# Kernel optimization log

Hardware: AMD Instinct MI355X
Metric: run time of the kernel (lower is better)

Reference implementation:

```python
import jax, jax.numpy as jnp
import numpy as np

# Grid config: output_shape = [2, 40, 400, 352, 16] -> sparse_shape = [41, 400, 352]
B, Dz, Hy, Wx = 2, 41, 400, 352
N_PER = 20000          # active voxels per sample
C_IN = 128
# Strided SparseConv3d(k=3, s=2, p=1) output spatial dims
Do, Ho, Wo = (Dz + 2 - 3) // 2 + 1, (Hy + 2 - 3) // 2 + 1, (Wx + 2 - 3) // 2 + 1


def setup_inputs() -> dict:
    rng = np.random.default_rng(0)
    coors_list = []
    for b in range(B):
        # unique voxel positions per sample (z limited to original 40-deep grid)
        flat = rng.choice((Dz - 1) * Hy * Wx, size=N_PER, replace=False)
        z = flat // (Hy * Wx)
        r = flat % (Hy * Wx)
        y = r // Wx
        x = r % Wx
        coors_list.append(np.stack([np.full(N_PER, b), z, y, x], axis=1))
    coors = jnp.asarray(np.concatenate(coors_list, 0), jnp.int32)  # [N,4]

    key = jax.random.key(0)
    k1, k2, k3, k4 = jax.random.split(key, 4)
    N = B * N_PER
    voxel_features = jax.random.normal(k1, (N, C_IN), jnp.float32)
    W1 = jax.random.normal(k2, (3, 3, 3, C_IN, 16), jnp.float32) * (1.0 / np.sqrt(27 * C_IN))
    W2 = jax.random.normal(k3, (3, 3, 3, 16, 16), jnp.float32) * (1.0 / np.sqrt(27 * 16))
    W3 = jax.random.normal(k4, (3, 3, 3, 16, 32), jnp.float32) * (1.0 / np.sqrt(27 * 16))
    return dict(voxel_features=voxel_features, coors=coors, W1=W1, W2=W2, W3=W3, batch_size=B)


def _offsets():
    o = jnp.stack(jnp.meshgrid(jnp.arange(3), jnp.arange(3), jnp.arange(3), indexing='ij'), -1)
    return o.reshape(27, 3)  # [27,3] kernel taps


def reference(voxel_features, coors, W1, W2, W3, batch_size):
    N = voxel_features.shape[0]
    offs = _offsets()

    # --- rulebook: dense index grid, padded by 1 so neighbor lookups never go OOB
    grid = jnp.full((batch_size, Dz + 2, Hy + 2, Wx + 2), -1, jnp.int32)
    grid = grid.at[coors[:, 0], coors[:, 1] + 1, coors[:, 2] + 1, coors[:, 3] + 1].set(
        jnp.arange(N, dtype=jnp.int32))
    # neighbor voxel index for every active site and every 3x3x3 tap: [N,27]
    nbr = grid[coors[:, 0:1], coors[:, 1:2] + offs[:, 0], coors[:, 2:3] + offs[:, 1],
               coors[:, 3:4] + offs[:, 2]]
    valid = (nbr >= 0)[..., None]
    nbr_c = jnp.clip(nbr, 0, N - 1)

    def subm(feat, W):  # submanifold conv: gather -> GEMM, output only on active sites
        Cin, Cout = W.shape[3], W.shape[4]
        g = jnp.where(valid, feat[nbr_c], 0.0)                      # [N,27,Cin]
        return jnp.einsum('nkc,kcd->nd', g, W.reshape(27, Cin, Cout))

    x = jax.nn.relu(subm(voxel_features, W1))   # SubMConv3d(128->16) + ReLU
    x = jax.nn.relu(subm(x, W2))                # SubMConv3d(16->16, same rulebook) + ReLU

    # --- SparseConv3d(16->32, k=3, stride=2, pad=1): scatter-add into downsampled grid
    contrib = jnp.einsum('nc,kcd->nkd', x, W3.reshape(27, 16, 32))  # [N,27,32]
    oz = coors[:, 1:2] + 1 - offs[:, 0]  # p_in + pad - k, must be even and in range
    oy = coors[:, 2:3] + 1 - offs[:, 1]
    ox = coors[:, 3:4] + 1 - offs[:, 2]
    pz, py, px = oz // 2, oy // 2, ox // 2
    ok = ((oz % 2 == 0) & (oy % 2 == 0) & (ox % 2 == 0) &
          (pz >= 0) & (pz < Do) & (py >= 0) & (py < Ho) & (px >= 0) & (px < Wo))
    total = batch_size * Do * Ho * Wo
    flat = coors[:, 0:1] * (Do * Ho * Wo) + pz * (Ho * Wo) + py * Wo + px
    flat = jnp.where(ok, flat, total)  # invalid -> dummy slot
    out = jnp.zeros((total + 1, 32), x.dtype).at[flat.reshape(-1)].add(
        contrib.reshape(-1, 32))[:total]
    out = jax.nn.relu(out).reshape(batch_size, Do, Ho, Wo, 32)  # dense() of sparse output
    return out
```

## Files before the change

### kernel.cpp

```cpp
#include <hip/hip_runtime.h>

#define B_   2
#define DZ   41
#define HY   400
#define WX   352
#define NVOX 40000
#define PD   43
#define PH   402
#define PW   354
#define DO_  21
#define HO_  200
#define WO_  176
#define C1   128
#define GRID_CELLS (B_*PD*PH*PW)
#define OUT_POS    (B_*DO_*HO_*WO_)
#define OUT_BYTES  ((size_t)OUT_POS * 32 * sizeof(float))


__global__ void k_build(const int* __restrict__ coors, unsigned short* __restrict__ grid) {
    int n = blockIdx.x * blockDim.x + threadIdx.x;
    if (n >= NVOX) return;
    int b = coors[4*n+0], z = coors[4*n+1], y = coors[4*n+2], x = coors[4*n+3];
    grid[((b*PD + z+1)*PH + y+1)*PW + x+1] = (unsigned short)(n + 1);
}

__global__ void k_nbr(const int* __restrict__ coors, const unsigned short* __restrict__ grid,
                      int* __restrict__ list, int* __restrict__ cnt) {
    int n = blockIdx.x * blockDim.x + threadIdx.x;
    if (n >= NVOX) return;
    int b = coors[4*n+0], z = coors[4*n+1], y = coors[4*n+2], x = coors[4*n+3];
    int c = 0;
    int* lp = list + n * 27;
    #pragma unroll
    for (int dz = 0; dz < 3; ++dz) {
        #pragma unroll
        for (int dy = 0; dy < 3; ++dy) {
            const unsigned short* row = grid + ((size_t)(b*PD + z + dz)*PH + (y + dy))*PW + x;
            #pragma unroll
            for (int dx = 0; dx < 3; ++dx) {
                int id = (int)row[dx] - 1;
                if (id >= 0) lp[c++] = ((dz*9 + dy*3 + dx) << 16) | id;
            }
        }
    }
    cnt[n] = c;
}

__global__ void k_subm1(const float* __restrict__ feat,
                        const float* __restrict__ W1,
                        const int* __restrict__ list, const int* __restrict__ cnt,
                        float* __restrict__ x1) {
    __shared__ int s_list[16][28];
    __shared__ int s_cnt[16];
    int base = blockIdx.x * 16;
    if (threadIdx.x < 16) {
        int n = base + threadIdx.x;
        s_cnt[threadIdx.x] = (n < NVOX) ? cnt[n] : 0;
    }
    for (int i = threadIdx.x; i < 16*27; i += 256) {
        int v = i / 27, k = i % 27;
        int n = base + v;
        s_list[v][k] = (n < NVOX) ? list[n*27 + k] : 0;
    }
    __syncthreads();
    int v = threadIdx.x >> 4, d = threadIdx.x & 15;
    int n = base + v;
    if (n >= NVOX) return;
    int m = s_cnt[v];
    float a0 = 0.f, a1 = 0.f, a2 = 0.f, a3 = 0.f;
    for (int t = 0; t < m; ++t) {
        int e = s_list[v][t];
        int k = e >> 16, idx = e & 0xFFFF;
        const float4* f4 = (const float4*)(feat + (size_t)idx * C1);
        const float* w = W1 + k * (C1*16) + d;
        #pragma unroll
        for (int c4 = 0; c4 < 32; ++c4) {
            float4 fv = f4[c4];
            const float* wp = w + c4 * 64;
            a0 += fv.x * wp[0];
            a1 += fv.y * wp[16];
            a2 += fv.z * wp[32];
            a3 += fv.w * wp[48];
        }
    }
    x1[n*16 + d] = fmaxf((a0 + a1) + (a2 + a3), 0.f);
}

__global__ void k_subm2(const float* __restrict__ x1,
                        const float* __restrict__ W2,
                        const int* __restrict__ list, const int* __restrict__ cnt,
                        float* __restrict__ x2) {
    __shared__ int   s_list[16][28];
    __shared__ int   s_cnt[16];
    __shared__ float s_w2[27*16*16];
    for (int i = threadIdx.x; i < 27*16*16; i += 256) s_w2[i] = W2[i];
    int base = blockIdx.x * 16;
    if (threadIdx.x < 16) {
        int n = base + threadIdx.x;
        s_cnt[threadIdx.x] = (n < NVOX) ? cnt[n] : 0;
    }
    for (int i = threadIdx.x; i < 16*27; i += 256) {
        int v = i / 27, k = i % 27;
        int n = base + v;
        s_list[v][k] = (n < NVOX) ? list[n*27 + k] : 0;
    }
    __syncthreads();
    int v = threadIdx.x >> 4, d = threadIdx.x & 15;
    int n = base + v;
    if (n >= NVOX) return;
    int m = s_cnt[v];
    float a0 = 0.f, a1 = 0.f, a2 = 0.f, a3 = 0.f;
    for (int t = 0; t < m; ++t) {
        int e = s_list[v][t];
        int k = e >> 16, idx = e & 0xFFFF;
        const float4* x4 = (const float4*)(x1 + (size_t)idx * 16);
        float4 xa = x4[0], xb = x4[1], xc = x4[2], xd = x4[3];
        const float* wp = s_w2 + k * 256 + d;
        a0 += xa.x * wp[0*16]  + xa.y * wp[1*16]  + xa.z * wp[2*16]  + xa.w * wp[3*16];
        a1 += xb.x * wp[4*16]  + xb.y * wp[5*16]  + xb.z * wp[6*16]  + xb.w * wp[7*16];
        a2 += xc.x * wp[8*16]  + xc.y * wp[9*16]  + xc.z * wp[10*16] + xc.w * wp[11*16];
        a3 += xd.x * wp[12*16] + xd.y * wp[13*16] + xd.z * wp[14*16] + xd.w * wp[15*16];
    }
    x2[n*16 + d] = fmaxf((a0 + a1) + (a2 + a3), 0.f);
}

__device__ __forceinline__ int axis_taps(int pcoord, int outdim, int* ds, int* ps) {
    if (pcoord & 1) { ds[0] = 1; ps[0] = pcoord >> 1; return 1; }
    int h = pcoord >> 1, nu = 0;
    if (h < outdim) { ds[nu] = 0; ps[nu] = h; nu++; }
    ds[nu] = 2; ps[nu] = h - 1; nu++;
    return nu;
}

__global__ void k_scatter(const float* __restrict__ x2,
                          const float* __restrict__ W3,
                          const int* __restrict__ coors,
                          float* __restrict__ out) {
    int v = threadIdx.x >> 5, d = threadIdx.x & 31;
    int n = blockIdx.x * 8 + v;
    if (n >= NVOX) return;
    int b  = coors[4*n+0];
    int zp = coors[4*n+1] + 1, yp = coors[4*n+2] + 1, xp = coors[4*n+3] + 1;
    int dz[2], pz[2], dy[2], py[2], dx[2], px[2];
    int nz = axis_taps(zp, DO_, dz, pz);
    int ny = axis_taps(yp, HO_, dy, py);
    int nx = axis_taps(xp, WO_, dx, px);
    const float4* xr = (const float4*)(x2 + (size_t)n * 16);
    float r[16];
    *(float4*)(r + 0)  = xr[0];
    *(float4*)(r + 4)  = xr[1];
    *(float4*)(r + 8)  = xr[2];
    *(float4*)(r + 12) = xr[3];
    int bofs = b * (DO_*HO_*WO_);
    for (int iz = 0; iz < nz; ++iz)
        for (int iy = 0; iy < ny; ++iy)
            for (int ix = 0; ix < nx; ++ix) {
                int k = dz[iz]*9 + dy[iy]*3 + dx[ix];
                int p = bofs + (pz[iz]*HO_ + py[iy])*WO_ + px[ix];
                const float* w = W3 + k*512 + d;
                float acc = 0.f;
                #pragma unroll
                for (int c = 0; c < 16; ++c) acc += r[c] * w[c * 32];
                atomicAdd(out + (size_t)p * 32 + d, acc);
            }
}

__global__ void k_relu(const int* __restrict__ coors, float* __restrict__ out) {
    int v = threadIdx.x >> 5, d = threadIdx.x & 31;
    int n = blockIdx.x * 8 + v;
    if (n >= NVOX) return;
    int b  = coors[4*n+0];
    int zp = coors[4*n+1] + 1, yp = coors[4*n+2] + 1, xp = coors[4*n+3] + 1;
    int dz[2], pz[2], dy[2], py[2], dx[2], px[2];
    int nz = axis_taps(zp, DO_, dz, pz);
    int ny = axis_taps(yp, HO_, dy, py);
    int nx = axis_taps(xp, WO_, dx, px);
    int bofs = b * (DO_*HO_*WO_);
    for (int iz = 0; iz < nz; ++iz)
        for (int iy = 0; iy < ny; ++iy)
            for (int ix = 0; ix < nx; ++ix) {
                int p = bofs + (pz[iz]*HO_ + py[iy])*WO_ + px[ix];
                size_t o = (size_t)p * 32 + d;
                out[o] = fmaxf(out[o], 0.f);
            }
}

extern "C" void kernel_launch(void* const* d_in, const int* in_sizes, int n_in,
                              void* d_out, int out_size, void* d_ws, size_t ws_size,
                              hipStream_t stream) {
    const float* feat  = (const float*)d_in[0];
    const int*   coors = (const int*)d_in[1];
    const float* W1    = (const float*)d_in[2];
    const float* W2    = (const float*)d_in[3];
    const float* W3    = (const float*)d_in[4];
    float* out = (float*)d_out;

    char* ws = (char*)d_ws;
    size_t off = 0;
    unsigned short* grid = (unsigned short*)(ws + off);
    off += (((size_t)GRID_CELLS*2) + 255) & ~(size_t)255;
    int* list = (int*)(ws + off); off += (((size_t)NVOX*27*4) + 255) & ~(size_t)255;
    int* cnt  = (int*)(ws + off); off += (((size_t)NVOX*4)    + 255) & ~(size_t)255;
    float* x1 = (float*)(ws + off); off += (((size_t)NVOX*16*4) + 255) & ~(size_t)255;
    float* x2 = (float*)(ws + off);

    hipMemsetAsync(grid, 0x00, (size_t)GRID_CELLS * 2, stream);
    hipMemsetAsync(out, 0x00, OUT_BYTES, stream);
    k_build<<<(NVOX + 255) / 256, 256, 0, stream>>>(coors, grid);
    k_nbr<<<(NVOX + 255) / 256, 256, 0, stream>>>(coors, grid, list, cnt);
    k_subm1<<<(NVOX + 15) / 16, 256, 0, stream>>>(feat, W1, list, cnt, x1);
    k_subm2<<<(NVOX + 15) / 16, 256, 0, stream>>>(x1, W2, list, cnt, x2);
    k_scatter<<<(NVOX + 7) / 8, 256, 0, stream>>>(x2, W3, coors, out);
    k_relu<<<(NVOX + 7) / 8, 256, 0, stream>>>(coors, out);
}
```

Before: 316.1 us.

## Transpose W1 for vectorized subm1 with wave-per-voxel split, flag-based ReLU pass

Adds a kernel that transposes W1 so each output channel's weights are contiguous, letting subm1 use float4 loads for both features and weights. Each 64-lane wave now handles one voxel, with four lane groups splitting the input channels and combining partial sums through shuffles. The ReLU pass is replaced by a flag bitmap written during the scatter, plus a kernel that scans every output position and applies ReLU only to flagged ones. This removes the redundant per-tap ReLU revisits, at the cost of an extra memset and a full pass over the flag array.

```diff
diff --git a/kernel.cpp b/kernel.cpp
--- a/kernel.cpp
+++ b/kernel.cpp
@@ -24,6 +24,13 @@
     grid[((b*PD + z+1)*PH + y+1)*PW + x+1] = (unsigned short)(n + 1);
 }
 
+__global__ void k_wtrans(const float* __restrict__ W1, float* __restrict__ W1t) {
+    int i = blockIdx.x * blockDim.x + threadIdx.x;
+    if (i >= 27*C1*16) return;
+    int k = i / (C1*16), r = i % (C1*16), c = r >> 4, d = r & 15;
+    W1t[(size_t)(k*16 + d)*C1 + c] = W1[i];
+}
+
 __global__ void k_nbr(const int* __restrict__ coors, const unsigned short* __restrict__ grid,
                       int* __restrict__ list, int* __restrict__ cnt) {
     int n = blockIdx.x * blockDim.x + threadIdx.x;
@@ -47,43 +54,34 @@
 }
 
 __global__ void k_subm1(const float* __restrict__ feat,
-                        const float* __restrict__ W1,
+                        const float* __restrict__ W1t,
                         const int* __restrict__ list, const int* __restrict__ cnt,
                         float* __restrict__ x1) {
-    __shared__ int s_list[16][28];
-    __shared__ int s_cnt[16];
-    int base = blockIdx.x * 16;
-    if (threadIdx.x < 16) {
-        int n = base + threadIdx.x;
-        s_cnt[threadIdx.x] = (n < NVOX) ? cnt[n] : 0;
-    }
-    for (int i = threadIdx.x; i < 16*27; i += 256) {
-        int v = i / 27, k = i % 27;
-        int n = base + v;
-        s_list[v][k] = (n < NVOX) ? list[n*27 + k] : 0;
-    }
-    __syncthreads();
-    int v = threadIdx.x >> 4, d = threadIdx.x & 15;
-    int n = base + v;
-    if (n >= NVOX) return;
-    int m = s_cnt[v];
+    int wid = (blockIdx.x * blockDim.x + threadIdx.x) >> 6;
+    int lane = threadIdx.x & 63;
+    if (wid >= NVOX) return;
+    int d = lane & 15, q = lane >> 4;
+    int m = cnt[wid];
+    const int* lp = list + wid * 27;
     float a0 = 0.f, a1 = 0.f, a2 = 0.f, a3 = 0.f;
     for (int t = 0; t < m; ++t) {
-        int e = s_list[v][t];
+        int e = lp[t];
         int k = e >> 16, idx = e & 0xFFFF;
-        const float4* f4 = (const float4*)(feat + (size_t)idx * C1);
-        const float* w = W1 + k * (C1*16) + d;
+        const float4* f4 = (const float4*)(feat + (size_t)idx * C1) + q*8;
+        const float4* w4 = (const float4*)(W1t + (size_t)(k*16 + d)*C1) + q*8;
         #pragma unroll
-        for (int c4 = 0; c4 < 32; ++c4) {
-            float4 fv = f4[c4];
-            const float* wp = w + c4 * 64;
-            a0 += fv.x * wp[0];
-            a1 += fv.y * wp[16];
-            a2 += fv.z * wp[32];
-            a3 += fv.w * wp[48];
+        for (int j = 0; j < 8; ++j) {
+            float4 fv = f4[j], wv = w4[j];
+            a0 += fv.x * wv.x;
+            a1 += fv.y * wv.y;
+            a2 += fv.z * wv.z;
+            a3 += fv.w * wv.w;
         }
     }
-    x1[n*16 + d] = fmaxf((a0 + a1) + (a2 + a3), 0.f);
+    float r = (a0 + a1) + (a2 + a3);
+    r += __shfl_xor(r, 16);
+    r += __shfl_xor(r, 32);
+    if (lane < 16) x1[wid*16 + d] = fmaxf(r, 0.f);
 }
 
 __global__ void k_subm2(const float* __restrict__ x1,
@@ -135,7 +133,8 @@
 __global__ void k_scatter(const float* __restrict__ x2,
                           const float* __restrict__ W3,
                           const int* __restrict__ coors,
-                          float* __restrict__ out) {
+                          float* __restrict__ out,
+                          unsigned char* __restrict__ flag) {
     int v = threadIdx.x >> 5, d = threadIdx.x & 31;
     int n = blockIdx.x * 8 + v;
     if (n >= NVOX) return;
@@ -162,27 +161,23 @@
                 #pragma unroll
                 for (int c = 0; c < 16; ++c) acc += r[c] * w[c * 32];
                 atomicAdd(out + (size_t)p * 32 + d, acc);
+                if (d == 0) flag[p] = 1;
             }
 }
 
-__global__ void k_relu(const int* __restrict__ coors, float* __restrict__ out) {
-    int v = threadIdx.x >> 5, d = threadIdx.x & 31;
-    int n = blockIdx.x * 8 + v;
-    if (n >= NVOX) return;
-    int b  = coors[4*n+0];
-    int zp = coors[4*n+1] + 1, yp = coors[4*n+2] + 1, xp = coors[4*n+3] + 1;
-    int dz[2], pz[2], dy[2], py[2], dx[2], px[2];
-    int nz = axis_taps(zp, DO_, dz, pz);
-    int ny = axis_taps(yp, HO_, dy, py);
-    int nx = axis_taps(xp, WO_, dx, px);
-    int bofs = b * (DO_*HO_*WO_);
-    for (int iz = 0; iz < nz; ++iz)
-        for (int iy = 0; iy < ny; ++iy)
-            for (int ix = 0; ix < nx; ++ix) {
-                int p = bofs + (pz[iz]*HO_ + py[iy])*WO_ + px[ix];
-                size_t o = (size_t)p * 32 + d;
-                out[o] = fmaxf(out[o], 0.f);
-            }
+__global__ void k_relu_flag(const unsigned char* __restrict__ flag,
+                            float* __restrict__ out) {
+    int p = blockIdx.x * blockDim.x + threadIdx.x;
+    if (p >= OUT_POS) return;
+    if (!flag[p]) return;
+    float4* o = (float4*)(out + (size_t)p * 32);
+    #pragma unroll
+    for (int j = 0; j < 8; ++j) {
+        float4 v = o[j];
+        v.x = fmaxf(v.x, 0.f); v.y = fmaxf(v.y, 0.f);
+        v.z = fmaxf(v.z, 0.f); v.w = fmaxf(v.w, 0.f);
+        o[j] = v;
+    }
 }
 
 extern "C" void kernel_launch(void* const* d_in, const int* in_sizes, int n_in,
@@ -202,14 +197,18 @@
     int* list = (int*)(ws + off); off += (((size_t)NVOX*27*4) + 255) & ~(size_t)255;
     int* cnt  = (int*)(ws + off); off += (((size_t)NVOX*4)    + 255) & ~(size_t)255;
     float* x1 = (float*)(ws + off); off += (((size_t)NVOX*16*4) + 255) & ~(size_t)255;
-    float* x2 = (float*)(ws + off);
+    float* x2 = (float*)(ws + off); off += (((size_t)NVOX*16*4) + 255) & ~(size_t)255;
+    float* W1t = (float*)(ws + off); off += (((size_t)27*C1*16*4) + 255) & ~(size_t)255;
+    unsigned char* flag = (unsigned char*)(ws + off); off += ((size_t)OUT_POS + 255) & ~(size_t)255;
 
     hipMemsetAsync(grid, 0x00, (size_t)GRID_CELLS * 2, stream);
+    hipMemsetAsync(flag, 0x00, (size_t)OUT_POS, stream);
     hipMemsetAsync(out, 0x00, OUT_BYTES, stream);
     k_build<<<(NVOX + 255) / 256, 256, 0, stream>>>(coors, grid);
+    k_wtrans<<<(27*C1*16 + 255) / 256, 256, 0, stream>>>(W1, W1t);
     k_nbr<<<(NVOX + 255) / 256, 256, 0, stream>>>(coors, grid, list, cnt);
-    k_subm1<<<(NVOX + 15) / 16, 256, 0, stream>>>(feat, W1, list, cnt, x1);
+    k_subm1<<<(NVOX*64 + 255) / 256, 256, 0, stream>>>(feat, W1t, list, cnt, x1);
     k_subm2<<<(NVOX + 15) / 16, 256, 0, stream>>>(x1, W2, list, cnt, x2);
-    k_scatter<<<(NVOX + 7) / 8, 256, 0, stream>>>(x2, W3, coors, out);
-    k_relu<<<(NVOX + 7) / 8, 256, 0, stream>>>(coors, out);
-}
+    k_scatter<<<(NVOX + 7) / 8, 256, 0, stream>>>(x2, W3, coors, out, flag);
+    k_relu_flag<<<(OUT_POS + 255) / 256, 256, 0, stream>>>(flag, out);
+}
```

New measurement: 327.1 us. +3.5%, slower.

## Fuse pipeline into one cooperative persistent kernel with grid syncs

Applied to the files above, without the earlier changes.

Merges grid clearing, output zeroing, rulebook build, neighbor search, both submanifold convs, the strided scatter and the final ReLU into one cooperative kernel separated by grid-wide syncs. The neighbor list is now built per 16-voxel chunk straight into shared memory and fed to the first conv, so it is not re-read from global memory there. The ReLU pass now walks a per-output-position flag array written during the scatter instead of recomputing taps per voxel. This is meant to remove launch and memset overheads and the list round trip, at the cost of grid syncs, a persistent grid limited by occupancy, and an extra byte-flag array that is cleared and scanned over all output positions.

```diff
diff --git a/kernel.cpp b/kernel.cpp
--- a/kernel.cpp
+++ b/kernel.cpp
@@ -1,4 +1,7 @@
 #include <hip/hip_runtime.h>
+#include <hip/hip_cooperative_groups.h>
+
+namespace cg = cooperative_groups;
 
 #define B_   2
 #define DZ   41
@@ -15,16 +18,186 @@
 #define GRID_CELLS (B_*PD*PH*PW)
 #define OUT_POS    (B_*DO_*HO_*WO_)
 #define OUT_BYTES  ((size_t)OUT_POS * 32 * sizeof(float))
-
-
-__global__ void k_build(const int* __restrict__ coors, unsigned short* __restrict__ grid) {
+#define NCHUNK     ((NVOX + 15) / 16)
+
+
+__device__ __forceinline__ int axis_taps(int pcoord, int outdim, int* ds, int* ps) {
+    if (pcoord & 1) { ds[0] = 1; ps[0] = pcoord >> 1; return 1; }
+    int h = pcoord >> 1, nu = 0;
+    if (h < outdim) { ds[nu] = 0; ps[nu] = h; nu++; }
+    ds[nu] = 2; ps[nu] = h - 1; nu++;
+    return nu;
+}
+
+__global__ void k_all(const float* __restrict__ feat, const int* __restrict__ coors,
+                      const float* __restrict__ W1, const float* __restrict__ W2,
+                      const float* __restrict__ W3,
+                      unsigned short* __restrict__ grid_, int* __restrict__ list,
+                      int* __restrict__ cnt, float* __restrict__ x1,
+                      float* __restrict__ x2, unsigned char* __restrict__ flag,
+                      float* __restrict__ out)
+{
+    cg::grid_group gg = cg::this_grid();
+    const int tid = blockIdx.x * blockDim.x + threadIdx.x;
+    const int gsz = gridDim.x * blockDim.x;
+
+    __shared__ int   s_list[16][28];
+    __shared__ int   s_cnt[16];
+    __shared__ float s_w2[27*256];
+
+    {
+        unsigned int* g32 = (unsigned int*)grid_;
+        for (int i = tid; i < GRID_CELLS/2; i += gsz) g32[i] = 0u;
+        float4 z4 = make_float4(0.f, 0.f, 0.f, 0.f);
+        float4* o4 = (float4*)out;
+        for (int i = tid; i < OUT_POS*8; i += gsz) o4[i] = z4;
+        unsigned int* fl = (unsigned int*)flag;
+        for (int i = tid; i < OUT_POS/4; i += gsz) fl[i] = 0u;
+    }
+    gg.sync();
+
+    for (int n = tid; n < NVOX; n += gsz) {
+        int b = coors[4*n+0], z = coors[4*n+1], y = coors[4*n+2], x = coors[4*n+3];
+        grid_[((b*PD + z+1)*PH + y+1)*PW + x+1] = (unsigned short)(n + 1);
+    }
+    gg.sync();
+
+    for (int cb = blockIdx.x; cb < NCHUNK; cb += gridDim.x) {
+        int base = cb * 16;
+        if (threadIdx.x < 16) {
+            int n = base + threadIdx.x;
+            int c = 0;
+            if (n < NVOX) {
+                int b = coors[4*n+0], z = coors[4*n+1], y = coors[4*n+2], x = coors[4*n+3];
+                #pragma unroll
+                for (int dz = 0; dz < 3; ++dz)
+                #pragma unroll
+                for (int dy = 0; dy < 3; ++dy) {
+                    const unsigned short* row = grid_ + ((size_t)(b*PD + z+dz)*PH + (y+dy))*PW + x;
+                    #pragma unroll
+                    for (int dx = 0; dx < 3; ++dx) {
+                        int id = (int)row[dx] - 1;
+                        if (id >= 0) s_list[threadIdx.x][c++] = ((dz*9 + dy*3 + dx) << 16) | id;
+                    }
+                }
+                cnt[n] = c;
+                for (int t = 0; t < c; ++t) list[n*27 + t] = s_list[threadIdx.x][t];
+            }
+            s_cnt[threadIdx.x] = c;
+        }
+        __syncthreads();
+        int v = threadIdx.x >> 4, d = threadIdx.x & 15;
+        int n = base + v;
+        if (n < NVOX) {
+            int m = s_cnt[v];
+            float a0 = 0.f, a1 = 0.f, a2 = 0.f, a3 = 0.f;
+            for (int t = 0; t < m; ++t) {
+                int e = s_list[v][t];
+                int k = e >> 16, idx = e & 0xFFFF;
+                const float4* f4 = (const float4*)(feat + (size_t)idx * C1);
+                const float* w = W1 + k * (C1*16) + d;
+                #pragma unroll
+                for (int c4 = 0; c4 < 32; ++c4) {
+                    float4 fv = f4[c4];
+                    const float* wp = w + c4 * 64;
+                    a0 += fv.x * wp[0];
+                    a1 += fv.y * wp[16];
+                    a2 += fv.z * wp[32];
+                    a3 += fv.w * wp[48];
+                }
+            }
+            x1[n*16 + d] = fmaxf((a0 + a1) + (a2 + a3), 0.f);
+        }
+        __syncthreads();
+    }
+    gg.sync();
+
+    for (int i = threadIdx.x; i < 27*256; i += blockDim.x) s_w2[i] = W2[i];
+    for (int cb = blockIdx.x; cb < NCHUNK; cb += gridDim.x) {
+        int base = cb * 16;
+        __syncthreads();
+        if (threadIdx.x < 16) {
+            int n = base + threadIdx.x;
+            s_cnt[threadIdx.x] = (n < NVOX) ? cnt[n] : 0;
+        }
+        for (int i = threadIdx.x; i < 16*27; i += blockDim.x) {
+            int v = i / 27, k = i % 27;
+            int n = base + v;
+            s_list[v][k] = (n < NVOX) ? list[n*27 + k] : 0;
+        }
+        __syncthreads();
+        int v = threadIdx.x >> 4, d = threadIdx.x & 15;
+        int n = base + v;
+        if (n < NVOX) {
+            int m = s_cnt[v];
+            float a0 = 0.f, a1 = 0.f, a2 = 0.f, a3 = 0.f;
+            for (int t = 0; t < m; ++t) {
+                int e = s_list[v][t];
+                int k = e >> 16, idx = e & 0xFFFF;
+                const float4* x4 = (const float4*)(x1 + (size_t)idx * 16);
+                float4 xa = x4[0], xb = x4[1], xc = x4[2], xd = x4[3];
+                const float* wp = s_w2 + k * 256 + d;
+                a0 += xa.x * wp[0*16]  + xa.y * wp[1*16]  + xa.z * wp[2*16]  + xa.w * wp[3*16];
+                a1 += xb.x * wp[4*16]  + xb.y * wp[5*16]  + xb.z * wp[6*16]  + xb.w * wp[7*16];
+                a2 += xc.x * wp[8*16]  + xc.y * wp[9*16]  + xc.z * wp[10*16] + xc.w * wp[11*16];
+                a3 += xd.x * wp[12*16] + xd.y * wp[13*16] + xd.z * wp[14*16] + xd.w * wp[15*16];
+            }
+            x2[n*16 + d] = fmaxf((a0 + a1) + (a2 + a3), 0.f);
+        }
+    }
+    gg.sync();
+
+    for (int nn = (tid >> 5); nn < NVOX; nn += (gsz >> 5)) {
+        int d = threadIdx.x & 31;
+        int b  = coors[4*nn+0];
+        int zp = coors[4*nn+1] + 1, yp = coors[4*nn+2] + 1, xp = coors[4*nn+3] + 1;
+        int dzv[2], pzv[2], dyv[2], pyv[2], dxv[2], pxv[2];
+        int nz = axis_taps(zp, DO_, dzv, pzv);
+        int ny = axis_taps(yp, HO_, dyv, pyv);
+        int nx = axis_taps(xp, WO_, dxv, pxv);
+        const float4* xr = (const float4*)(x2 + (size_t)nn * 16);
+        float r[16];
+        *(float4*)(r + 0)  = xr[0];
+        *(float4*)(r + 4)  = xr[1];
+        *(float4*)(r + 8)  = xr[2];
+        *(float4*)(r + 12) = xr[3];
+        int bofs = b * (DO_*HO_*WO_);
+        for (int iz = 0; iz < nz; ++iz)
+            for (int iy = 0; iy < ny; ++iy)
+                for (int ix = 0; ix < nx; ++ix) {
+                    int k = dzv[iz]*9 + dyv[iy]*3 + dxv[ix];
+                    int p = bofs + (pzv[iz]*HO_ + pyv[iy])*WO_ + pxv[ix];
+                    const float* w = W3 + k*512 + d;
+                    float acc = 0.f;
+                    #pragma unroll
+                    for (int c = 0; c < 16; ++c) acc += r[c] * w[c * 32];
+                    atomicAdd(out + (size_t)p * 32 + d, acc);
+                    if (d == 0) flag[p] = 1;
+                }
+    }
+    gg.sync();
+
+    for (int p = tid; p < OUT_POS; p += gsz) {
+        if (!flag[p]) continue;
+        float4* o = (float4*)(out + (size_t)p * 32);
+        #pragma unroll
+        for (int j = 0; j < 8; ++j) {
+            float4 vv = o[j];
+            vv.x = fmaxf(vv.x, 0.f); vv.y = fmaxf(vv.y, 0.f);
+            vv.z = fmaxf(vv.z, 0.f); vv.w = fmaxf(vv.w, 0.f);
+            o[j] = vv;
+        }
+    }
+}
+
+__global__ void k_build(const int* __restrict__ coors, unsigned short* __restrict__ grid_) {
     int n = blockIdx.x * blockDim.x + threadIdx.x;
     if (n >= NVOX) return;
     int b = coors[4*n+0], z = coors[4*n+1], y = coors[4*n+2], x = coors[4*n+3];
-    grid[((b*PD + z+1)*PH + y+1)*PW + x+1] = (unsigned short)(n + 1);
-}
-
-__global__ void k_nbr(const int* __restrict__ coors, const unsigned short* __restrict__ grid,
+    grid_[((b*PD + z+1)*PH + y+1)*PW + x+1] = (unsigned short)(n + 1);
+}
+
+__global__ void k_nbr(const int* __restrict__ coors, const unsigned short* __restrict__ grid_,
                       int* __restrict__ list, int* __restrict__ cnt) {
     int n = blockIdx.x * blockDim.x + threadIdx.x;
     if (n >= NVOX) return;
@@ -32,22 +205,20 @@
     int c = 0;
     int* lp = list + n * 27;
     #pragma unroll
-    for (int dz = 0; dz < 3; ++dz) {
+    for (int dz = 0; dz < 3; ++dz)
+    #pragma unroll
+    for (int dy = 0; dy < 3; ++dy) {
+        const unsigned short* row = grid_ + ((size_t)(b*PD + z+dz)*PH + (y+dy))*PW + x;
         #pragma unroll
-        for (int dy = 0; dy < 3; ++dy) {
-            const unsigned short* row = grid + ((size_t)(b*PD + z + dz)*PH + (y + dy))*PW + x;
-            #pragma unroll
-            for (int dx = 0; dx < 3; ++dx) {
-                int id = (int)row[dx] - 1;
-                if (id >= 0) lp[c++] = ((dz*9 + dy*3 + dx) << 16) | id;
-            }
+        for (int dx = 0; dx < 3; ++dx) {
+            int id = (int)row[dx] - 1;
+            if (id >= 0) lp[c++] = ((dz*9 + dy*3 + dx) << 16) | id;
         }
     }
     cnt[n] = c;
 }
 
-__global__ void k_subm1(const float* __restrict__ feat,
-                        const float* __restrict__ W1,
+__global__ void k_subm1(const float* __restrict__ feat, const float* __restrict__ W1,
                         const int* __restrict__ list, const int* __restrict__ cnt,
                         float* __restrict__ x1) {
     __shared__ int s_list[16][28];
@@ -77,23 +248,20 @@
         for (int c4 = 0; c4 < 32; ++c4) {
             float4 fv = f4[c4];
             const float* wp = w + c4 * 64;
-            a0 += fv.x * wp[0];
-            a1 += fv.y * wp[16];
-            a2 += fv.z * wp[32];
-            a3 += fv.w * wp[48];
+            a0 += fv.x * wp[0]; a1 += fv.y * wp[16];
+            a2 += fv.z * wp[32]; a3 += fv.w * wp[48];
         }
     }
     x1[n*16 + d] = fmaxf((a0 + a1) + (a2 + a3), 0.f);
 }
 
-__global__ void k_subm2(const float* __restrict__ x1,
-                        const float* __restrict__ W2,
+__global__ void k_subm2(const float* __restrict__ x1, const float* __restrict__ W2,
                         const int* __restrict__ list, const int* __restrict__ cnt,
                         float* __restrict__ x2) {
     __shared__ int   s_list[16][28];
     __shared__ int   s_cnt[16];
-    __shared__ float s_w2[27*16*16];
-    for (int i = threadIdx.x; i < 27*16*16; i += 256) s_w2[i] = W2[i];
+    __shared__ float s_w2[27*256];
+    for (int i = threadIdx.x; i < 27*256; i += 256) s_w2[i] = W2[i];
     int base = blockIdx.x * 16;
     if (threadIdx.x < 16) {
         int n = base + threadIdx.x;
@@ -124,27 +292,18 @@
     x2[n*16 + d] = fmaxf((a0 + a1) + (a2 + a3), 0.f);
 }
 
-__device__ __forceinline__ int axis_taps(int pcoord, int outdim, int* ds, int* ps) {
-    if (pcoord & 1) { ds[0] = 1; ps[0] = pcoord >> 1; return 1; }
-    int h = pcoord >> 1, nu = 0;
-    if (h < outdim) { ds[nu] = 0; ps[nu] = h; nu++; }
-    ds[nu] = 2; ps[nu] = h - 1; nu++;
-    return nu;
-}
-
-__global__ void k_scatter(const float* __restrict__ x2,
-                          const float* __restrict__ W3,
-                          const int* __restrict__ coors,
-                          float* __restrict__ out) {
+__global__ void k_scatter(const float* __restrict__ x2, const float* __restrict__ W3,
+                          const int* __restrict__ coors, float* __restrict__ out,
+                          unsigned char* __restrict__ flag) {
     int v = threadIdx.x >> 5, d = threadIdx.x & 31;
     int n = blockIdx.x * 8 + v;
     if (n >= NVOX) return;
     int b  = coors[4*n+0];
     int zp = coors[4*n+1] + 1, yp = coors[4*n+2] + 1, xp = coors[4*n+3] + 1;
-    int dz[2], pz[2], dy[2], py[2], dx[2], px[2];
-    int nz = axis_taps(zp, DO_, dz, pz);
-    int ny = axis_taps(yp, HO_, dy, py);
-    int nx = axis_taps(xp, WO_, dx, px);
+    int dzv[2], pzv[2], dyv[2], pyv[2], dxv[2], pxv[2];
+    int nz = axis_taps(zp, DO_, dzv, pzv);
+    int ny = axis_taps(yp, HO_, dyv, pyv);
+    int nx = axis_taps(xp, WO_, dxv, pxv);
     const float4* xr = (const float4*)(x2 + (size_t)n * 16);
     float r[16];
     *(float4*)(r + 0)  = xr[0];
@@ -155,34 +314,29 @@
     for (int iz = 0; iz < nz; ++iz)
         for (int iy = 0; iy < ny; ++iy)
             for (int ix = 0; ix < nx; ++ix) {
-                int k = dz[iz]*9 + dy[iy]*3 + dx[ix];
-                int p = bofs + (pz[iz]*HO_ + py[iy])*WO_ + px[ix];
+                int k = dzv[iz]*9 + dyv[iy]*3 + dxv[ix];
+                int p = bofs + (pzv[iz]*HO_ + pyv[iy])*WO_ + pxv[ix];
                 const float* w = W3 + k*512 + d;
                 float acc = 0.f;
                 #pragma unroll
                 for (int c = 0; c < 16; ++c) acc += r[c] * w[c * 32];
                 atomicAdd(out + (size_t)p * 32 + d, acc);
+                if (d == 0) flag[p] = 1;
             }
 }
 
-__global__ void k_relu(const int* __restrict__ coors, float* __restrict__ out) {
-    int v = threadIdx.x >> 5, d = threadIdx.x & 31;
-    int n = blockIdx.x * 8 + v;
-    if (n >= NVOX) return;
-    int b  = coors[4*n+0];
-    int zp = coors[4*n+1] + 1, yp = coors[4*n+2] + 1, xp = coors[4*n+3] + 1;
-    int dz[2], pz[2], dy[2], py[2], dx[2], px[2];
-    int nz = axis_taps(zp, DO_, dz, pz);
-    int ny = axis_taps(yp, HO_, dy, py);
-    int nx = axis_taps(xp, WO_, dx, px);
-    int bofs = b * (DO_*HO_*WO_);
-    for (int iz = 0; iz < nz; ++iz)
-        for (int iy = 0; iy < ny; ++iy)
-            for (int ix = 0; ix < nx; ++ix) {
-                int p = bofs + (pz[iz]*HO_ + py[iy])*WO_ + px[ix];
-                size_t o = (size_t)p * 32 + d;
-                out[o] = fmaxf(out[o], 0.f);
-            }
+__global__ void k_relu_flag(const unsigned char* __restrict__ flag, float* __restrict__ out) {
+    int p = blockIdx.x * blockDim.x + threadIdx.x;
+    if (p >= OUT_POS) return;
+    if (!flag[p]) return;
+    float4* o = (float4*)(out + (size_t)p * 32);
+    #pragma unroll
+    for (int j = 0; j < 8; ++j) {
+        float4 v = o[j];
+        v.x = fmaxf(v.x, 0.f); v.y = fmaxf(v.y, 0.f);
+        v.z = fmaxf(v.z, 0.f); v.w = fmaxf(v.w, 0.f);
+        o[j] = v;
+    }
 }
 
 extern "C" void kernel_launch(void* const* d_in, const int* in_sizes, int n_in,
@@ -202,14 +356,36 @@
     int* list = (int*)(ws + off); off += (((size_t)NVOX*27*4) + 255) & ~(size_t)255;
     int* cnt  = (int*)(ws + off); off += (((size_t)NVOX*4)    + 255) & ~(size_t)255;
     float* x1 = (float*)(ws + off); off += (((size_t)NVOX*16*4) + 255) & ~(size_t)255;
-    float* x2 = (float*)(ws + off);
-
-    hipMemsetAsync(grid, 0x00, (size_t)GRID_CELLS * 2, stream);
-    hipMemsetAsync(out, 0x00, OUT_BYTES, stream);
-    k_build<<<(NVOX + 255) / 256, 256, 0, stream>>>(coors, grid);
-    k_nbr<<<(NVOX + 255) / 256, 256, 0, stream>>>(coors, grid, list, cnt);
-    k_subm1<<<(NVOX + 15) / 16, 256, 0, stream>>>(feat, W1, list, cnt, x1);
-    k_subm2<<<(NVOX + 15) / 16, 256, 0, stream>>>(x1, W2, list, cnt, x2);
-    k_scatter<<<(NVOX + 7) / 8, 256, 0, stream>>>(x2, W3, coors, out);
-    k_relu<<<(NVOX + 7) / 8, 256, 0, stream>>>(coors, out);
-}
+    float* x2 = (float*)(ws + off); off += (((size_t)NVOX*16*4) + 255) & ~(size_t)255;
+    unsigned char* flag = (unsigned char*)(ws + off); off += ((size_t)OUT_POS + 255) & ~(size_t)255;
+
+    static int coop_blocks = -2;
+    if (coop_blocks == -2) {
+        int per_cu = 0;
+        hipError_t e = hipOccupancyMaxActiveBlocksPerMultiprocessor(&per_cu, k_all, 256, 0);
+        coop_blocks = (e == hipSuccess && per_cu >= 1) ? per_cu * 256 : -1;
+    }
+
+    bool ok = false;
+    if (coop_blocks > 0) {
+        void* args[] = { (void*)&feat, (void*)&coors, (void*)&W1, (void*)&W2, (void*)&W3,
+                         (void*)&grid, (void*)&list, (void*)&cnt, (void*)&x1, (void*)&x2,
+                         (void*)&flag, (void*)&out };
+        hipError_t e = hipLaunchCooperativeKernel((const void*)k_all, dim3(coop_blocks),
+                                                  dim3(256), args, 0, stream);
+        ok = (e == hipSuccess);
+        if (!ok) coop_blocks = -1;
+    }
+
+    if (!ok) {
+        hipMemsetAsync(grid, 0x00, (size_t)GRID_CELLS * 2, stream);
+        hipMemsetAsync(flag, 0x00, (size_t)OUT_POS, stream);
+        hipMemsetAsync(out, 0x00, OUT_BYTES, stream);
+        k_build<<<(NVOX + 255) / 256, 256, 0, stream>>>(coors, grid);
+        k_nbr<<<(NVOX + 255) / 256, 256, 0, stream>>>(coors, grid, list, cnt);
+        k_subm1<<<(NVOX + 15) / 16, 256, 0, stream>>>(feat, W1, list, cnt, x1);
+        k_subm2<<<(NVOX + 15) / 16, 256, 0, stream>>>(x1, W2, list, cnt, x2);
+        k_scatter<<<(NVOX + 7) / 8, 256, 0, stream>>>(x2, W3, coors, out, flag);
+        k_relu_flag<<<(OUT_POS + 255) / 256, 256, 0, stream>>>(flag, out);
+    }
+}
```

Result: slower. 672.1 us (+112.6%).

## Fuse neighbor search into subm1, transpose weights, replace output memset with flag-based finalize

Applied to the files above, without the earlier changes.

The output memset is replaced by zeroing only the touched output positions inside the fused neighbor/subm1 kernel. A final pass writes zeros to untouched positions and applies ReLU to touched ones, using a byte flag per output position. W1 and W3 are transposed in the build kernel so each thread reads contiguous float4 weights, and the separate k_nbr and k_relu kernels are folded away. The finalize pass still writes the full dense output, and the flag array adds a memset and byte reads.

```diff
diff --git a/kernel.cpp b/kernel.cpp
--- a/kernel.cpp
+++ b/kernel.cpp
@@ -14,86 +14,120 @@
 #define C1   128
 #define GRID_CELLS (B_*PD*PH*PW)
 #define OUT_POS    (B_*DO_*HO_*WO_)
-#define OUT_BYTES  ((size_t)OUT_POS * 32 * sizeof(float))
-
-
-__global__ void k_build(const int* __restrict__ coors, unsigned short* __restrict__ grid) {
-    int n = blockIdx.x * blockDim.x + threadIdx.x;
-    if (n >= NVOX) return;
-    int b = coors[4*n+0], z = coors[4*n+1], y = coors[4*n+2], x = coors[4*n+3];
-    grid[((b*PD + z+1)*PH + y+1)*PW + x+1] = (unsigned short)(n + 1);
-}
-
-__global__ void k_nbr(const int* __restrict__ coors, const unsigned short* __restrict__ grid,
-                      int* __restrict__ list, int* __restrict__ cnt) {
-    int n = blockIdx.x * blockDim.x + threadIdx.x;
-    if (n >= NVOX) return;
-    int b = coors[4*n+0], z = coors[4*n+1], y = coors[4*n+2], x = coors[4*n+3];
-    int c = 0;
-    int* lp = list + n * 27;
-    #pragma unroll
-    for (int dz = 0; dz < 3; ++dz) {
-        #pragma unroll
-        for (int dy = 0; dy < 3; ++dy) {
-            const unsigned short* row = grid + ((size_t)(b*PD + z + dz)*PH + (y + dy))*PW + x;
-            #pragma unroll
-            for (int dx = 0; dx < 3; ++dx) {
-                int id = (int)row[dx] - 1;
-                if (id >= 0) lp[c++] = ((dz*9 + dy*3 + dx) << 16) | id;
-            }
-        }
-    }
-    cnt[n] = c;
-}
-
-__global__ void k_subm1(const float* __restrict__ feat,
-                        const float* __restrict__ W1,
-                        const int* __restrict__ list, const int* __restrict__ cnt,
-                        float* __restrict__ x1) {
+#define NCHUNK     ((NVOX + 15) / 16)
+#define W1_ELEMS   (27*C1*16)
+#define W3_ELEMS   (27*16*32)
+
+
+__device__ __forceinline__ int axis_taps(int pcoord, int outdim, int* ds, int* ps) {
+    if (pcoord & 1) { ds[0] = 1; ps[0] = pcoord >> 1; return 1; }
+    int h = pcoord >> 1, nu = 0;
+    if (h < outdim) { ds[nu] = 0; ps[nu] = h; nu++; }
+    ds[nu] = 2; ps[nu] = h - 1; nu++;
+    return nu;
+}
+
+__global__ void k_build(const int* __restrict__ coors,
+                        const float* __restrict__ W1, const float* __restrict__ W3,
+                        unsigned short* __restrict__ grid_,
+                        float* __restrict__ W1t, float* __restrict__ W3t) {
+    int i = blockIdx.x * blockDim.x + threadIdx.x;
+    if (i < NVOX) {
+        int b = coors[4*i+0], z = coors[4*i+1], y = coors[4*i+2], x = coors[4*i+3];
+        grid_[((b*PD + z+1)*PH + y+1)*PW + x+1] = (unsigned short)(i + 1);
+    } else if (i < NVOX + W1_ELEMS) {
+        int j = i - NVOX;
+        int k = j >> 11, r = j & 2047, c = r >> 4, d = r & 15;
+        W1t[((size_t)k*16 + d)*C1 + c] = W1[j];
+    } else if (i < NVOX + W1_ELEMS + W3_ELEMS) {
+        int j = i - NVOX - W1_ELEMS;
+        int k = j >> 9, r = j & 511, c = r >> 5, d = r & 31;
+        W3t[((size_t)k*32 + d)*16 + c] = W3[j];
+    }
+}
+
+__global__ void k_nbr_subm1(const float* __restrict__ feat, const int* __restrict__ coors,
+                            const unsigned short* __restrict__ grid_,
+                            const float* __restrict__ W1t,
+                            int* __restrict__ list, int* __restrict__ cnt,
+                            float* __restrict__ x1,
+                            unsigned char* __restrict__ flag, float* __restrict__ out) {
     __shared__ int s_list[16][28];
     __shared__ int s_cnt[16];
+    __shared__ int s_pos[16][8];
+    __shared__ int s_np[16];
     int base = blockIdx.x * 16;
     if (threadIdx.x < 16) {
         int n = base + threadIdx.x;
-        s_cnt[threadIdx.x] = (n < NVOX) ? cnt[n] : 0;
-    }
-    for (int i = threadIdx.x; i < 16*27; i += 256) {
-        int v = i / 27, k = i % 27;
-        int n = base + v;
-        s_list[v][k] = (n < NVOX) ? list[n*27 + k] : 0;
+        int c = 0, np = 0;
+        if (n < NVOX) {
+            int b = coors[4*n+0], z = coors[4*n+1], y = coors[4*n+2], x = coors[4*n+3];
+            #pragma unroll
+            for (int dz = 0; dz < 3; ++dz)
+            #pragma unroll
+            for (int dy = 0; dy < 3; ++dy) {
+                const unsigned short* row = grid_ + ((size_t)(b*PD + z+dz)*PH + (y+dy))*PW + x;
+                #pragma unroll
+                for (int dx = 0; dx < 3; ++dx) {
+                    int id = (int)row[dx] - 1;
+                    if (id >= 0) s_list[threadIdx.x][c++] = ((dz*9 + dy*3 + dx) << 16) | id;
+                }
+            }
+            cnt[n] = c;
+            int* lp = list + n * 27;
+            for (int t = 0; t < c; ++t) lp[t] = s_list[threadIdx.x][t];
+            int zp = z + 1, yp = y + 1, xp = x + 1;
+            int dzv[2], pzv[2], dyv[2], pyv[2], dxv[2], pxv[2];
+            int nz = axis_taps(zp, DO_, dzv, pzv);
+            int ny = axis_taps(yp, HO_, dyv, pyv);
+            int nx = axis_taps(xp, WO_, dxv, pxv);
+            int bofs = b * (DO_*HO_*WO_);
+            for (int iz = 0; iz < nz; ++iz)
+                for (int iy = 0; iy < ny; ++iy)
+                    for (int ix = 0; ix < nx; ++ix) {
+                        int p = bofs + (pzv[iz]*HO_ + pyv[iy])*WO_ + pxv[ix];
+                        s_pos[threadIdx.x][np++] = p;
+                        flag[p] = 1;
+                    }
+        }
+        s_cnt[threadIdx.x] = c;
+        s_np[threadIdx.x]  = np;
     }
     __syncthreads();
     int v = threadIdx.x >> 4, d = threadIdx.x & 15;
     int n = base + v;
     if (n >= NVOX) return;
+    int np = s_np[v];
+    for (int t = 0; t < np; ++t) {
+        int p = s_pos[v][t];
+        ((float2*)(out + (size_t)p * 32))[d] = make_float2(0.f, 0.f);
+    }
     int m = s_cnt[v];
     float a0 = 0.f, a1 = 0.f, a2 = 0.f, a3 = 0.f;
     for (int t = 0; t < m; ++t) {
         int e = s_list[v][t];
         int k = e >> 16, idx = e & 0xFFFF;
         const float4* f4 = (const float4*)(feat + (size_t)idx * C1);
-        const float* w = W1 + k * (C1*16) + d;
+        const float4* w4 = (const float4*)(W1t + ((size_t)k*16 + d)*C1);
         #pragma unroll
         for (int c4 = 0; c4 < 32; ++c4) {
-            float4 fv = f4[c4];
-            const float* wp = w + c4 * 64;
-            a0 += fv.x * wp[0];
-            a1 += fv.y * wp[16];
-            a2 += fv.z * wp[32];
-            a3 += fv.w * wp[48];
+            float4 fv = f4[c4], wv = w4[c4];
+            a0 += fv.x * wv.x;
+            a1 += fv.y * wv.y;
+            a2 += fv.z * wv.z;
+            a3 += fv.w * wv.w;
         }
     }
     x1[n*16 + d] = fmaxf((a0 + a1) + (a2 + a3), 0.f);
 }
 
-__global__ void k_subm2(const float* __restrict__ x1,
-                        const float* __restrict__ W2,
+__global__ void k_subm2(const float* __restrict__ x1, const float* __restrict__ W2,
                         const int* __restrict__ list, const int* __restrict__ cnt,
                         float* __restrict__ x2) {
     __shared__ int   s_list[16][28];
     __shared__ int   s_cnt[16];
-    __shared__ float s_w2[27*16*16];
-    for (int i = threadIdx.x; i < 27*16*16; i += 256) s_w2[i] = W2[i];
+    __shared__ float s_w2[27*256];
+    for (int i = threadIdx.x; i < 27*256; i += 256) s_w2[i] = W2[i];
     int base = blockIdx.x * 16;
     if (threadIdx.x < 16) {
         int n = base + threadIdx.x;
@@ -124,65 +158,52 @@
     x2[n*16 + d] = fmaxf((a0 + a1) + (a2 + a3), 0.f);
 }
 
-__device__ __forceinline__ int axis_taps(int pcoord, int outdim, int* ds, int* ps) {
-    if (pcoord & 1) { ds[0] = 1; ps[0] = pcoord >> 1; return 1; }
-    int h = pcoord >> 1, nu = 0;
-    if (h < outdim) { ds[nu] = 0; ps[nu] = h; nu++; }
-    ds[nu] = 2; ps[nu] = h - 1; nu++;
-    return nu;
-}
-
-__global__ void k_scatter(const float* __restrict__ x2,
-                          const float* __restrict__ W3,
-                          const int* __restrict__ coors,
-                          float* __restrict__ out) {
+__global__ void k_scatter(const float* __restrict__ x2, const float* __restrict__ W3t,
+                          const int* __restrict__ coors, float* __restrict__ out) {
     int v = threadIdx.x >> 5, d = threadIdx.x & 31;
     int n = blockIdx.x * 8 + v;
     if (n >= NVOX) return;
     int b  = coors[4*n+0];
     int zp = coors[4*n+1] + 1, yp = coors[4*n+2] + 1, xp = coors[4*n+3] + 1;
-    int dz[2], pz[2], dy[2], py[2], dx[2], px[2];
-    int nz = axis_taps(zp, DO_, dz, pz);
-    int ny = axis_taps(yp, HO_, dy, py);
-    int nx = axis_taps(xp, WO_, dx, px);
+    int dzv[2], pzv[2], dyv[2], pyv[2], dxv[2], pxv[2];
+    int nz = axis_taps(zp, DO_, dzv, pzv);
+    int ny = axis_taps(yp, HO_, dyv, pyv);
+    int nx = axis_taps(xp, WO_, dxv, pxv);
     const float4* xr = (const float4*)(x2 + (size_t)n * 16);
-    float r[16];
-    *(float4*)(r + 0)  = xr[0];
-    *(float4*)(r + 4)  = xr[1];
-    *(float4*)(r + 8)  = xr[2];
-    *(float4*)(r + 12) = xr[3];
+    float4 r0 = xr[0], r1 = xr[1], r2 = xr[2], r3 = xr[3];
     int bofs = b * (DO_*HO_*WO_);
     for (int iz = 0; iz < nz; ++iz)
         for (int iy = 0; iy < ny; ++iy)
             for (int ix = 0; ix < nx; ++ix) {
-                int k = dz[iz]*9 + dy[iy]*3 + dx[ix];
-                int p = bofs + (pz[iz]*HO_ + py[iy])*WO_ + px[ix];
-                const float* w = W3 + k*512 + d;
-                float acc = 0.f;
-                #pragma unroll
-                for (int c = 0; c < 16; ++c) acc += r[c] * w[c * 32];
+                int k = dzv[iz]*9 + dyv[iy]*3 + dxv[ix];
+                int p = bofs + (pzv[iz]*HO_ + pyv[iy])*WO_ + pxv[ix];
+                const float4* w4 = (const float4*)(W3t + ((size_t)k*32 + d)*16);
+                float4 w0 = w4[0], w1 = w4[1], w2 = w4[2], w3 = w4[3];
+                float acc = r0.x*w0.x + r0.y*w0.y + r0.z*w0.z + r0.w*w0.w
+                          + r1.x*w1.x + r1.y*w1.y + r1.z*w1.z + r1.w*w1.w
+                          + r2.x*w2.x + r2.y*w2.y + r2.z*w2.z + r2.w*w2.w
+                          + r3.x*w3.x + r3.y*w3.y + r3.z*w3.z + r3.w*w3.w;
                 atomicAdd(out + (size_t)p * 32 + d, acc);
             }
 }
 
-__global__ void k_relu(const int* __restrict__ coors, float* __restrict__ out) {
-    int v = threadIdx.x >> 5, d = threadIdx.x & 31;
-    int n = blockIdx.x * 8 + v;
-    if (n >= NVOX) return;
-    int b  = coors[4*n+0];
-    int zp = coors[4*n+1] + 1, yp = coors[4*n+2] + 1, xp = coors[4*n+3] + 1;
-    int dz[2], pz[2], dy[2], py[2], dx[2], px[2];
-    int nz = axis_taps(zp, DO_, dz, pz);
-    int ny = axis_taps(yp, HO_, dy, py);
-    int nx = axis_taps(xp, WO_, dx, px);
-    int bofs = b * (DO_*HO_*WO_);
-    for (int iz = 0; iz < nz; ++iz)
-        for (int iy = 0; iy < ny; ++iy)
-            for (int ix = 0; ix < nx; ++ix) {
-                int p = bofs + (pz[iz]*HO_ + py[iy])*WO_ + px[ix];
-                size_t o = (size_t)p * 32 + d;
-                out[o] = fmaxf(out[o], 0.f);
-            }
+__global__ void k_finalize(const unsigned char* __restrict__ flag, float* __restrict__ out) {
+    int p = blockIdx.x * blockDim.x + threadIdx.x;
+    if (p >= OUT_POS) return;
+    float4* o = (float4*)(out + (size_t)p * 32);
+    if (flag[p]) {
+        #pragma unroll
+        for (int j = 0; j < 8; ++j) {
+            float4 v = o[j];
+            v.x = fmaxf(v.x, 0.f); v.y = fmaxf(v.y, 0.f);
+            v.z = fmaxf(v.z, 0.f); v.w = fmaxf(v.w, 0.f);
+            o[j] = v;
+        }
+    } else {
+        float4 z = make_float4(0.f, 0.f, 0.f, 0.f);
+        #pragma unroll
+        for (int j = 0; j < 8; ++j) o[j] = z;
+    }
 }
 
 extern "C" void kernel_launch(void* const* d_in, const int* in_sizes, int n_in,
@@ -199,17 +220,21 @@
     size_t off = 0;
     unsigned short* grid = (unsigned short*)(ws + off);
     off += (((size_t)GRID_CELLS*2) + 255) & ~(size_t)255;
+    unsigned char* flag = (unsigned char*)(ws + off);
+    off += ((size_t)OUT_POS + 255) & ~(size_t)255;
+    size_t zero_span = off;
     int* list = (int*)(ws + off); off += (((size_t)NVOX*27*4) + 255) & ~(size_t)255;
     int* cnt  = (int*)(ws + off); off += (((size_t)NVOX*4)    + 255) & ~(size_t)255;
     float* x1 = (float*)(ws + off); off += (((size_t)NVOX*16*4) + 255) & ~(size_t)255;
-    float* x2 = (float*)(ws + off);
-
-    hipMemsetAsync(grid, 0x00, (size_t)GRID_CELLS * 2, stream);
-    hipMemsetAsync(out, 0x00, OUT_BYTES, stream);
-    k_build<<<(NVOX + 255) / 256, 256, 0, stream>>>(coors, grid);
-    k_nbr<<<(NVOX + 255) / 256, 256, 0, stream>>>(coors, grid, list, cnt);
-    k_subm1<<<(NVOX + 15) / 16, 256, 0, stream>>>(feat, W1, list, cnt, x1);
-    k_subm2<<<(NVOX + 15) / 16, 256, 0, stream>>>(x1, W2, list, cnt, x2);
-    k_scatter<<<(NVOX + 7) / 8, 256, 0, stream>>>(x2, W3, coors, out);
-    k_relu<<<(NVOX + 7) / 8, 256, 0, stream>>>(coors, out);
-}
+    float* x2 = (float*)(ws + off); off += (((size_t)NVOX*16*4) + 255) & ~(size_t)255;
+    float* W1t = (float*)(ws + off); off += (((size_t)W1_ELEMS*4) + 255) & ~(size_t)255;
+    float* W3t = (float*)(ws + off); off += (((size_t)W3_ELEMS*4) + 255) & ~(size_t)255;
+
+    hipMemsetAsync(ws, 0x00, zero_span, stream);
+    k_build<<<(NVOX + W1_ELEMS + W3_ELEMS + 255) / 256, 256, 0, stream>>>(
+        coors, W1, W3, grid, W1t, W3t);
+    k_nbr_subm1<<<NCHUNK, 256, 0, stream>>>(feat, coors, grid, W1t, list, cnt, x1, flag, out);
+    k_subm2<<<NCHUNK, 256, 0, stream>>>(x1, W2, list, cnt, x2);
+    k_scatter<<<(NVOX + 7) / 8, 256, 0, stream>>>(x2, W3t, coors, out);
+    k_finalize<<<(OUT_POS + 255) / 256, 256, 0, stream>>>(flag, out);
+}
```

Result: slower. 349.5 us (+10.6%).
